# Kernel optimization log

Hardware: AMD Instinct MI355X
Metric: run time of the kernel (lower is better)

The kernel has to match this reference:

```python
import jax, jax.numpy as jnp
import numpy as np

N = 4096
IN_F = 512
OUT_F = 512


def setup_inputs() -> dict:
    key = jax.random.key(0)
    k1, k2, k3, k4 = jax.random.split(key, 4)
    x = jax.random.normal(k1, (N, IN_F), dtype=jnp.float32)
    adj = jax.random.uniform(k2, (N, N), dtype=jnp.float32)
    # linear params (torch nn.Linear default init: U(-1/sqrt(fan_in), 1/sqrt(fan_in)))
    bound = 1.0 / np.sqrt(IN_F)
    W = jax.random.uniform(k3, (OUT_F, IN_F), minval=-bound, maxval=bound, dtype=jnp.float32)
    b = jax.random.uniform(k4, (OUT_F,), minval=-bound, maxval=bound, dtype=jnp.float32)
    return {"x": x, "adj": adj, "W": W, "b": b}


def reference(x, adj, W, b):
    # adj_hat = adj + I
    adj_hat = adj + jnp.eye(adj.shape[0], dtype=adj.dtype)
    # deg is diagonal with 1/sqrt(rowsum); deg @ adj @ deg == d[:,None] * adj * d[None,:]
    d = 1.0 / jnp.sqrt(adj_hat.sum(axis=1))  # [N]
    norm_adj = d[:, None] * adj_hat * d[None, :]  # [N, N]
    h = norm_adj @ x  # [N, in_features]
    return h @ W.T + b  # [N, out_features]
```

## Files before the change

### kernel.cpp

```cpp
#include <hip/hip_runtime.h>
#include <cstdint>

#define NN 4096
#define FF 512

typedef short bf16x8 __attribute__((ext_vector_type(8)));
typedef float f32x4 __attribute__((ext_vector_type(4)));

__device__ __forceinline__ uint16_t f2bf(float f) {
    uint32_t u = __builtin_bit_cast(uint32_t, f);
    u += 0x7FFFu + ((u >> 16) & 1u);
    return (uint16_t)(u >> 16);
}

__global__ __launch_bounds__(256) void k_prep(const float* __restrict__ adj,
                                              float* __restrict__ d,
                                              uint16_t* __restrict__ Abf) {
    const int row  = blockIdx.x * 4 + (threadIdx.x >> 6);
    const int lane = threadIdx.x & 63;
    const float4* p = (const float4*)(adj + (size_t)row * NN);
    float4 v[16];
    float s = 0.f;
#pragma unroll
    for (int i = 0; i < 16; ++i) {
        v[i] = p[lane + i * 64];
        s += (v[i].x + v[i].y) + (v[i].z + v[i].w);
    }
#pragma unroll
    for (int off = 1; off < 64; off <<= 1) s += __shfl_xor(s, off);
    const float di = rsqrtf(s + 1.0f);
    if (lane == 0) d[row] = di;
    uint16_t* outp = Abf + (size_t)row * NN;
#pragma unroll
    for (int i = 0; i < 16; ++i) {
        const int cb = (lane + i * 64) * 4;
        float a0 = v[i].x * di, a1 = v[i].y * di, a2 = v[i].z * di, a3 = v[i].w * di;
        if (cb + 0 == row) a0 += di;
        if (cb + 1 == row) a1 += di;
        if (cb + 2 == row) a2 += di;
        if (cb + 3 == row) a3 += di;
        ushort4 o;
        o.x = f2bf(a0); o.y = f2bf(a1); o.z = f2bf(a2); o.w = f2bf(a3);
        *(ushort4*)(outp + cb) = o;
    }
}

__global__ __launch_bounds__(256) void k_xt(const float* __restrict__ x,
                                            const float* __restrict__ d,
                                            uint16_t* __restrict__ yT) {
    __shared__ uint16_t t[64][72];
    const int k0 = blockIdx.x * 64;
    const int n0 = blockIdx.y * 64;
    const int tid = threadIdx.x;
    const int r   = tid >> 4;
    const int c4  = tid & 15;
#pragma unroll
    for (int pass = 0; pass < 4; ++pass) {
        const int row = pass * 16 + r;
        float4 v = *(const float4*)(x + (size_t)(k0 + row) * FF + n0 + c4 * 4);
        const float dk = d[k0 + row];
        t[c4 * 4 + 0][row] = f2bf(v.x * dk);
        t[c4 * 4 + 1][row] = f2bf(v.y * dk);
        t[c4 * 4 + 2][row] = f2bf(v.z * dk);
        t[c4 * 4 + 3][row] = f2bf(v.w * dk);
    }
    __syncthreads();
#pragma unroll
    for (int pass = 0; pass < 2; ++pass) {
        const int cid = pass * 256 + tid;
        const int n  = cid >> 3;
        const int ch = cid & 7;
        *(uint4*)(yT + (size_t)(n0 + n) * NN + k0 + ch * 8) = *(const uint4*)&t[n][ch * 8];
    }
}

__global__ __launch_bounds__(256) void k_wc(const float* __restrict__ W,
                                            uint16_t* __restrict__ Wbf) {
    const size_t t4 = (size_t)blockIdx.x * 256 + threadIdx.x;
    float4 v = *(const float4*)(W + t4 * 4);
    ushort4 o;
    o.x = f2bf(v.x); o.y = f2bf(v.y); o.z = f2bf(v.z); o.w = f2bf(v.w);
    *(ushort4*)(Wbf + t4 * 4) = o;
}

template <int K, bool OUT_BF16>
__global__ __launch_bounds__(256, 2) void k_gemm(const uint16_t* __restrict__ A,
                                                 const uint16_t* __restrict__ Bt,
                                                 const float* __restrict__ bias,
                                                 uint16_t* __restrict__ outb,
                                                 float* __restrict__ outf) {
    __shared__ uint16_t As[64 * 64];
    __shared__ uint16_t Bs[64 * 64];

    const int id   = blockIdx.x;
    const int xcd  = id & 7;
    const int slot = id >> 3;
    const int n_t  = slot & 7;
    const int m_t  = xcd * 8 + (slot >> 3);
    const int m0 = m_t * 64;
    const int n0 = n_t * 64;

    const int tid  = threadIdx.x;
    const int w    = tid >> 6;
    const int lane = tid & 63;
    const int wm = w >> 1, wn = w & 1;

    f32x4 acc[2][2] = {};

    for (int kt = 0; kt < K / 64; ++kt) {
        __syncthreads();
#pragma unroll
        for (int i = 0; i < 2; ++i) {
            const int boff = w * 2048 + i * 1024 + lane * 16;
            const int row  = boff >> 7;
            const int q    = (boff >> 4) & 7;
            const int c    = q ^ (row & 7);
            const uint16_t* srcA = A  + (size_t)(m0 + row) * K + kt * 64 + c * 8;
            const uint16_t* srcB = Bt + (size_t)(n0 + row) * K + kt * 64 + c * 8;
            __builtin_amdgcn_global_load_lds(
                (const __attribute__((address_space(1))) void*)srcA,
                (__attribute__((address_space(3))) void*)&As[(w * 2048 + i * 1024) >> 1],
                16, 0, 0);
            __builtin_amdgcn_global_load_lds(
                (const __attribute__((address_space(1))) void*)srcB,
                (__attribute__((address_space(3))) void*)&Bs[(w * 2048 + i * 1024) >> 1],
                16, 0, 0);
        }
        __syncthreads();

#pragma unroll
        for (int kk = 0; kk < 2; ++kk) {
            bf16x8 af[2], bfr[2];
#pragma unroll
            for (int mf = 0; mf < 2; ++mf) {
                const int m  = wm * 32 + mf * 16 + (lane & 15);
                const int ch = (kk * 4 + (lane >> 4)) ^ (m & 7);
                af[mf] = *(const bf16x8*)&As[m * 64 + ch * 8];
            }
#pragma unroll
            for (int nf = 0; nf < 2; ++nf) {
                const int n  = wn * 32 + nf * 16 + (lane & 15);
                const int ch = (kk * 4 + (lane >> 4)) ^ (n & 7);
                bfr[nf] = *(const bf16x8*)&Bs[n * 64 + ch * 8];
            }
#pragma unroll
            for (int mf = 0; mf < 2; ++mf)
#pragma unroll
                for (int nf = 0; nf < 2; ++nf)
                    acc[mf][nf] = __builtin_amdgcn_mfma_f32_16x16x32_bf16(
                        af[mf], bfr[nf], acc[mf][nf], 0, 0, 0);
        }
    }

#pragma unroll
    for (int mf = 0; mf < 2; ++mf) {
#pragma unroll
        for (int nf = 0; nf < 2; ++nf) {
            const int rbase = m0 + wm * 32 + mf * 16 + ((lane >> 4) << 2);
            const int col   = n0 + wn * 32 + nf * 16 + (lane & 15);
#pragma unroll
            for (int r = 0; r < 4; ++r) {
                const size_t idx = (size_t)(rbase + r) * FF + col;
                if constexpr (OUT_BF16) {
                    outb[idx] = f2bf(acc[mf][nf][r]);
                } else {
                    outf[idx] = acc[mf][nf][r] + bias[col];
                }
            }
        }
    }
}

extern "C" void kernel_launch(void* const* d_in, const int* in_sizes, int n_in,
                              void* d_out, int out_size, void* d_ws, size_t ws_size,
                              hipStream_t stream) {
    const float* x   = (const float*)d_in[0];
    const float* adj = (const float*)d_in[1];
    const float* W   = (const float*)d_in[2];
    const float* b   = (const float*)d_in[3];
    float* out = (float*)d_out;

    char* ws = (char*)d_ws;
    float*    d_   = (float*)ws;
    uint16_t* Abf  = (uint16_t*)(ws + 65536);
    uint16_t* yT   = Abf + (size_t)NN * NN;
    uint16_t* hbf  = yT  + (size_t)FF * NN;
    uint16_t* Wbf  = hbf + (size_t)NN * FF;

    k_prep<<<NN / 4, 256, 0, stream>>>(adj, d_, Abf);
    k_xt<<<dim3(NN / 64, FF / 64), 256, 0, stream>>>(x, d_, yT);
    k_wc<<<FF * FF / 4 / 256, 256, 0, stream>>>(W, Wbf);
    k_gemm<NN, true><<<(NN / 64) * (FF / 64), 256, 0, stream>>>(Abf, yT, nullptr, hbf, nullptr);
    k_gemm<FF, false><<<(NN / 64) * (FF / 64), 256, 0, stream>>>(hbf, Wbf, b, nullptr, out);
}
```

Measured before the change: 71.62 us.

## Add 4-stage LDS pipeline with async prefetch to bf16 GEMM

Replaces the single-buffered load/sync/compute loop with a four-buffer ring. Each tile is prefetched three iterations ahead via global_load_lds, and explicit vmcnt waits plus barriers gate the compute, so global-memory latency overlaps with MFMA work. LDS use grows from 16KB to 64KB per block. With launch_bounds(256,2) this may cap occupancy, and the hand-counted vmcnt values must match the number of issued loads.

```diff
diff --git a/kernel.cpp b/kernel.cpp
--- a/kernel.cpp
+++ b/kernel.cpp
@@ -89,8 +89,9 @@
                                                  const float* __restrict__ bias,
                                                  uint16_t* __restrict__ outb,
                                                  float* __restrict__ outf) {
-    __shared__ uint16_t As[64 * 64];
-    __shared__ uint16_t Bs[64 * 64];
+    constexpr int NT = K / 64;
+    __shared__ uint16_t As[4][64 * 64];
+    __shared__ uint16_t Bs[4][64 * 64];
 
     const int id   = blockIdx.x;
     const int xcd  = id & 7;
@@ -107,27 +108,27 @@
 
     f32x4 acc[2][2] = {};
 
-    for (int kt = 0; kt < K / 64; ++kt) {
-        __syncthreads();
+    auto STAGE = [&](int t, int buf) {
 #pragma unroll
         for (int i = 0; i < 2; ++i) {
             const int boff = w * 2048 + i * 1024 + lane * 16;
             const int row  = boff >> 7;
             const int q    = (boff >> 4) & 7;
             const int c    = q ^ (row & 7);
-            const uint16_t* srcA = A  + (size_t)(m0 + row) * K + kt * 64 + c * 8;
-            const uint16_t* srcB = Bt + (size_t)(n0 + row) * K + kt * 64 + c * 8;
+            const uint16_t* srcA = A  + (size_t)(m0 + row) * K + t * 64 + c * 8;
+            const uint16_t* srcB = Bt + (size_t)(n0 + row) * K + t * 64 + c * 8;
             __builtin_amdgcn_global_load_lds(
                 (const __attribute__((address_space(1))) void*)srcA,
-                (__attribute__((address_space(3))) void*)&As[(w * 2048 + i * 1024) >> 1],
+                (__attribute__((address_space(3))) void*)&As[buf][(w * 2048 + i * 1024) >> 1],
                 16, 0, 0);
             __builtin_amdgcn_global_load_lds(
                 (const __attribute__((address_space(1))) void*)srcB,
-                (__attribute__((address_space(3))) void*)&Bs[(w * 2048 + i * 1024) >> 1],
+                (__attribute__((address_space(3))) void*)&Bs[buf][(w * 2048 + i * 1024) >> 1],
                 16, 0, 0);
         }
-        __syncthreads();
-
+    };
+
+    auto COMPUTE = [&](int buf) {
 #pragma unroll
         for (int kk = 0; kk < 2; ++kk) {
             bf16x8 af[2], bfr[2];
@@ -135,13 +136,13 @@
             for (int mf = 0; mf < 2; ++mf) {
                 const int m  = wm * 32 + mf * 16 + (lane & 15);
                 const int ch = (kk * 4 + (lane >> 4)) ^ (m & 7);
-                af[mf] = *(const bf16x8*)&As[m * 64 + ch * 8];
+                af[mf] = *(const bf16x8*)&As[buf][m * 64 + ch * 8];
             }
 #pragma unroll
             for (int nf = 0; nf < 2; ++nf) {
                 const int n  = wn * 32 + nf * 16 + (lane & 15);
                 const int ch = (kk * 4 + (lane >> 4)) ^ (n & 7);
-                bfr[nf] = *(const bf16x8*)&Bs[n * 64 + ch * 8];
+                bfr[nf] = *(const bf16x8*)&Bs[buf][n * 64 + ch * 8];
             }
 #pragma unroll
             for (int mf = 0; mf < 2; ++mf)
@@ -150,7 +151,28 @@
                     acc[mf][nf] = __builtin_amdgcn_mfma_f32_16x16x32_bf16(
                         af[mf], bfr[nf], acc[mf][nf], 0, 0, 0);
         }
-    }
+    };
+
+    STAGE(0, 0);
+    STAGE(1, 1);
+    STAGE(2, 2);
+
+    for (int t = 0; t < NT - 3; ++t) {
+        STAGE(t + 3, (t + 3) & 3);
+        asm volatile("s_waitcnt vmcnt(12)" ::: "memory");
+        __builtin_amdgcn_s_barrier();
+        COMPUTE(t & 3);
+        __builtin_amdgcn_s_barrier();
+    }
+    asm volatile("s_waitcnt vmcnt(8)" ::: "memory");
+    __builtin_amdgcn_s_barrier();
+    COMPUTE((NT - 3) & 3);
+    asm volatile("s_waitcnt vmcnt(4)" ::: "memory");
+    __builtin_amdgcn_s_barrier();
+    COMPUTE((NT - 2) & 3);
+    asm volatile("s_waitcnt vmcnt(0)" ::: "memory");
+    __builtin_amdgcn_s_barrier();
+    COMPUTE((NT - 1) & 3);
 
 #pragma unroll
     for (int mf = 0; mf < 2; ++mf) {
```

Measured after the change: 69.98 us. 1.02x faster.

## Use 128-row tiles, 32x32 MFMA, double-buffered LDS, and split-K for the big GEMM

Applied to the files above, without the earlier changes.

Rewrites the GEMM kernel to use larger 128xBN tiles with 32x32x16 MFMA instructions and double-buffered LDS staging, with explicit vmcnt waits so global loads overlap compute. The big N×N×F GEMM uses split-K=2 with fp32 atomicAdd into a zeroed buffer, then a separate conversion kernel produces bf16 h. The goal is better data reuse per block and latency hiding, while keeping enough blocks for occupancy. In exchange it adds a memset, atomic traffic, an extra kernel pass over h, and reduced occupancy from the launch bounds and larger LDS.

```diff
diff --git a/kernel.cpp b/kernel.cpp
--- a/kernel.cpp
+++ b/kernel.cpp
@@ -5,7 +5,7 @@
 #define FF 512
 
 typedef short bf16x8 __attribute__((ext_vector_type(8)));
-typedef float f32x4 __attribute__((ext_vector_type(4)));
+typedef float f32x16 __attribute__((ext_vector_type(16)));
 
 __device__ __forceinline__ uint16_t f2bf(float f) {
     uint32_t u = __builtin_bit_cast(uint32_t, f);
@@ -83,88 +83,126 @@
     *(ushort4*)(Wbf + t4 * 4) = o;
 }
 
-template <int K, bool OUT_BF16>
-__global__ __launch_bounds__(256, 2) void k_gemm(const uint16_t* __restrict__ A,
+__global__ __launch_bounds__(256) void k_cvt(const float* __restrict__ h32,
+                                             uint16_t* __restrict__ hbf) {
+    const size_t t4 = (size_t)blockIdx.x * 256 + threadIdx.x;
+    float4 v = *(const float4*)(h32 + t4 * 4);
+    ushort4 o;
+    o.x = f2bf(v.x); o.y = f2bf(v.y); o.z = f2bf(v.z); o.w = f2bf(v.w);
+    *(ushort4*)(hbf + t4 * 4) = o;
+}
+
+template <int K, int SPLITK, int NF, int MODE>
+__global__ __launch_bounds__(256, 1) void k_gemm(const uint16_t* __restrict__ A,
                                                  const uint16_t* __restrict__ Bt,
                                                  const float* __restrict__ bias,
-                                                 uint16_t* __restrict__ outb,
                                                  float* __restrict__ outf) {
-    __shared__ uint16_t As[64 * 64];
-    __shared__ uint16_t Bs[64 * 64];
-
-    const int id   = blockIdx.x;
-    const int xcd  = id & 7;
-    const int slot = id >> 3;
-    const int n_t  = slot & 7;
-    const int m_t  = xcd * 8 + (slot >> 3);
-    const int m0 = m_t * 64;
-    const int n0 = n_t * 64;
+    constexpr int KS = K / SPLITK;
+    constexpr int NT = KS / 64;
+    constexpr int BN = 64 * NF;
+    constexpr int NTIL = 512 / BN;
+    __shared__ uint16_t As[2][128 * 64];
+    __shared__ uint16_t Bs[2][BN * 64];
+
+    const int id  = blockIdx.x;
+    const int xcd = id & 7;
+    const int j   = id >> 3;
+    const int mt  = ((j / (NTIL * SPLITK)) << 3) | xcd;
+    const int rem = j % (NTIL * SPLITK);
+    const int nt  = rem / SPLITK;
+    const int ks  = rem % SPLITK;
+    const int m0 = mt * 128;
+    const int n0 = nt * BN;
+    const int k0 = ks * KS;
 
     const int tid  = threadIdx.x;
     const int w    = tid >> 6;
     const int lane = tid & 63;
     const int wm = w >> 1, wn = w & 1;
 
-    f32x4 acc[2][2] = {};
-
-    for (int kt = 0; kt < K / 64; ++kt) {
-        __syncthreads();
-#pragma unroll
-        for (int i = 0; i < 2; ++i) {
-            const int boff = w * 2048 + i * 1024 + lane * 16;
+    f32x16 acc[2][NF] = {};
+
+    auto STAGE = [&](int t, int buf) {
+        const int ktb = k0 + t * 64;
+#pragma unroll
+        for (int i = 0; i < 4; ++i) {
+            const int boff = i * 4096 + tid * 16;
             const int row  = boff >> 7;
             const int q    = (boff >> 4) & 7;
             const int c    = q ^ (row & 7);
-            const uint16_t* srcA = A  + (size_t)(m0 + row) * K + kt * 64 + c * 8;
-            const uint16_t* srcB = Bt + (size_t)(n0 + row) * K + kt * 64 + c * 8;
+            const uint16_t* src = A + (size_t)(m0 + row) * K + ktb + c * 8;
             __builtin_amdgcn_global_load_lds(
-                (const __attribute__((address_space(1))) void*)srcA,
-                (__attribute__((address_space(3))) void*)&As[(w * 2048 + i * 1024) >> 1],
+                (const __attribute__((address_space(1))) void*)src,
+                (__attribute__((address_space(3))) void*)&As[buf][i * 2048 + w * 512],
                 16, 0, 0);
+        }
+#pragma unroll
+        for (int i = 0; i < NF * 2; ++i) {
+            const int boff = i * 4096 + tid * 16;
+            const int row  = boff >> 7;
+            const int q    = (boff >> 4) & 7;
+            const int c    = q ^ (row & 7);
+            const uint16_t* src = Bt + (size_t)(n0 + row) * K + ktb + c * 8;
             __builtin_amdgcn_global_load_lds(
-                (const __attribute__((address_space(1))) void*)srcB,
-                (__attribute__((address_space(3))) void*)&Bs[(w * 2048 + i * 1024) >> 1],
+                (const __attribute__((address_space(1))) void*)src,
+                (__attribute__((address_space(3))) void*)&Bs[buf][i * 2048 + w * 512],
                 16, 0, 0);
         }
-        __syncthreads();
-
-#pragma unroll
-        for (int kk = 0; kk < 2; ++kk) {
-            bf16x8 af[2], bfr[2];
+    };
+
+    auto COMPUTE = [&](int buf) {
+#pragma unroll
+        for (int ksl = 0; ksl < 4; ++ksl) {
+            const int cl = ksl * 2 + (lane >> 5);
+            bf16x8 af[2], bfr[NF];
 #pragma unroll
             for (int mf = 0; mf < 2; ++mf) {
-                const int m  = wm * 32 + mf * 16 + (lane & 15);
-                const int ch = (kk * 4 + (lane >> 4)) ^ (m & 7);
-                af[mf] = *(const bf16x8*)&As[m * 64 + ch * 8];
+                const int r = wm * 64 + mf * 32 + (lane & 31);
+                af[mf] = *(const bf16x8*)&As[buf][r * 64 + ((cl ^ (r & 7)) << 3)];
             }
 #pragma unroll
-            for (int nf = 0; nf < 2; ++nf) {
-                const int n  = wn * 32 + nf * 16 + (lane & 15);
-                const int ch = (kk * 4 + (lane >> 4)) ^ (n & 7);
-                bfr[nf] = *(const bf16x8*)&Bs[n * 64 + ch * 8];
+            for (int nf = 0; nf < NF; ++nf) {
+                const int r = wn * (32 * NF) + nf * 32 + (lane & 31);
+                bfr[nf] = *(const bf16x8*)&Bs[buf][r * 64 + ((cl ^ (r & 7)) << 3)];
             }
 #pragma unroll
             for (int mf = 0; mf < 2; ++mf)
 #pragma unroll
-                for (int nf = 0; nf < 2; ++nf)
-                    acc[mf][nf] = __builtin_amdgcn_mfma_f32_16x16x32_bf16(
+                for (int nf = 0; nf < NF; ++nf)
+                    acc[mf][nf] = __builtin_amdgcn_mfma_f32_32x32x16_bf16(
                         af[mf], bfr[nf], acc[mf][nf], 0, 0, 0);
         }
-    }
+    };
+
+    STAGE(0, 0);
+    for (int t = 0; t < NT - 1; ++t) {
+        STAGE(t + 1, (t + 1) & 1);
+        if constexpr (NF == 2) asm volatile("s_waitcnt vmcnt(8)" ::: "memory");
+        else                   asm volatile("s_waitcnt vmcnt(6)" ::: "memory");
+        __builtin_amdgcn_s_barrier();
+        COMPUTE(t & 1);
+        __builtin_amdgcn_s_barrier();
+    }
+    asm volatile("s_waitcnt vmcnt(0)" ::: "memory");
+    __builtin_amdgcn_s_barrier();
+    COMPUTE((NT - 1) & 1);
 
 #pragma unroll
     for (int mf = 0; mf < 2; ++mf) {
 #pragma unroll
-        for (int nf = 0; nf < 2; ++nf) {
-            const int rbase = m0 + wm * 32 + mf * 16 + ((lane >> 4) << 2);
-            const int col   = n0 + wn * 32 + nf * 16 + (lane & 15);
-#pragma unroll
-            for (int r = 0; r < 4; ++r) {
-                const size_t idx = (size_t)(rbase + r) * FF + col;
-                if constexpr (OUT_BF16) {
-                    outb[idx] = f2bf(acc[mf][nf][r]);
+        for (int nf = 0; nf < NF; ++nf) {
+            const int gcol = n0 + wn * (32 * NF) + nf * 32 + (lane & 31);
+            const int rb   = m0 + wm * 64 + mf * 32 + ((lane >> 5) << 2);
+            float bv = 0.f;
+            if constexpr (MODE == 1) bv = bias[gcol];
+#pragma unroll
+            for (int r = 0; r < 16; ++r) {
+                const int grow = rb + (r & 3) + ((r >> 2) << 3);
+                const size_t idx = (size_t)grow * FF + gcol;
+                if constexpr (MODE == 0) {
+                    atomicAdd(&outf[idx], acc[mf][nf][r]);
                 } else {
-                    outf[idx] = acc[mf][nf][r] + bias[col];
+                    outf[idx] = acc[mf][nf][r] + bv;
                 }
             }
         }
@@ -186,10 +224,13 @@
     uint16_t* yT   = Abf + (size_t)NN * NN;
     uint16_t* hbf  = yT  + (size_t)FF * NN;
     uint16_t* Wbf  = hbf + (size_t)NN * FF;
-
+    float*    h32  = (float*)(Wbf + (size_t)FF * FF);
+
+    hipMemsetAsync(h32, 0, (size_t)NN * FF * sizeof(float), stream);
     k_prep<<<NN / 4, 256, 0, stream>>>(adj, d_, Abf);
     k_xt<<<dim3(NN / 64, FF / 64), 256, 0, stream>>>(x, d_, yT);
     k_wc<<<FF * FF / 4 / 256, 256, 0, stream>>>(W, Wbf);
-    k_gemm<NN, true><<<(NN / 64) * (FF / 64), 256, 0, stream>>>(Abf, yT, nullptr, hbf, nullptr);
-    k_gemm<FF, false><<<(NN / 64) * (FF / 64), 256, 0, stream>>>(hbf, Wbf, b, nullptr, out);
-}
+    k_gemm<NN, 2, 2, 0><<<256, 256, 0, stream>>>(Abf, yT, nullptr, h32);
+    k_cvt<<<NN * FF / 4 / 256, 256, 0, stream>>>(h32, hbf);
+    k_gemm<FF, 1, 1, 1><<<256, 256, 0, stream>>>(hbf, Wbf, b, out);
+}
```

Measured after the change: 84.46 us. 1.18x slower.
